# Performance work log

Measured on AMD Instinct MI355X. Metric: run time of the kernel, lower is better.

The kernel has to match this reference:

```python
import jax, jax.numpy as jnp
import numpy as np

KERNEL_MUL = 10.0
KERNEL_NUM = 5


def _multi_kernel(dist, n_samples):
    # bandwidth estimated from detached distances (torch uses .data)
    bw = jax.lax.stop_gradient(jnp.sum(dist)) / (n_samples * n_samples - n_samples)
    bw = bw / (KERNEL_MUL ** (KERNEL_NUM // 2))
    k = jnp.zeros_like(dist)
    for i in range(KERNEL_NUM):
        k = k + jnp.exp(-dist / (bw * KERNEL_MUL ** i))
    return k


def setup_inputs() -> dict:
    key = jax.random.key(0)
    k1, k2 = jax.random.split(key)
    B, D = 256, 512
    source = jax.random.normal(k1, (B, D), dtype=jnp.float32)
    target = jax.random.normal(k2, (B, D), dtype=jnp.float32)
    return {"source": source, "target": target}


def reference(source, target):
    B = source.shape[0]
    src = source.reshape(B, -1)
    tgt = target.reshape(target.shape[0], -1)
    total = jnp.concatenate([src, tgt], axis=0)  # [N, D], N = 2B
    N = total.shape[0]

    # L2 pairwise distances via norm expansion (avoids [N,N,D] intermediate)
    sq = jnp.sum(total * total, axis=1)  # [N]
    L2 = jnp.maximum(sq[:, None] + sq[None, :] - 2.0 * (total @ total.T), 0.0)

    # L1 pairwise distances (structurally needs pairwise diffs)
    L1 = jnp.sum(jnp.abs(total[:, None, :] - total[None, :, :]), axis=-1)  # [N, N]

    kernels = _multi_kernel(L2, N) + _multi_kernel(L1, N)

    XX = kernels[:B, :B]
    YY = kernels[B:, B:]
    XY = kernels[:B, B:]
    YX = kernels[B:, :B]
    return jnp.mean(XX + YY - XY - YX)
```

## Files before the change

### kernel.cpp

```cpp
#include <hip/hip_runtime.h>
#include <hip/hip_fp16.h>

#define NROWS 512
#define BHALF 256
#define DIM   512
#define TILE  64
#define DCHUNK 64
#define NCHUNK 8
#define NN (NROWS * NROWS)
#define SOFF (8 * NN)

#define ACC(A, Bb, IV, JV)                                    \
    {                                                         \
        const float d_ = (IV) - (JV);                         \
        a2[A][Bb] = fmaf(d_, d_, a2[A][Bb]);                  \
        a1[A][Bb] += fabsf(d_);                               \
    }

#define STEP(DD)                                              \
    {                                                         \
        const float4 ivv = *(const float4*)&ai[DD][ty4];      \
        const float4 jvv = *(const float4*)&aj[DD][tx4];      \
        ACC(0, 0, ivv.x, jvv.x) ACC(0, 1, ivv.x, jvv.y)       \
        ACC(0, 2, ivv.x, jvv.z) ACC(0, 3, ivv.x, jvv.w)       \
        ACC(1, 0, ivv.y, jvv.x) ACC(1, 1, ivv.y, jvv.y)       \
        ACC(1, 2, ivv.y, jvv.z) ACC(1, 3, ivv.y, jvv.w)       \
        ACC(2, 0, ivv.z, jvv.x) ACC(2, 1, ivv.z, jvv.y)       \
        ACC(2, 2, ivv.z, jvv.z) ACC(2, 3, ivv.z, jvv.w)       \
        ACC(3, 0, ivv.w, jvv.x) ACC(3, 1, ivv.w, jvv.y)       \
        ACC(3, 2, ivv.w, jvv.z) ACC(3, 3, ivv.w, jvv.w)       \
    }

__device__ __forceinline__ unsigned int pack_h2(float l2v, float l1v) {
    const __half2 h = __halves2half2(__float2half_rn(l2v), __float2half_rn(l1v));
    union { __half2 h; unsigned int u; } c; c.h = h;
    return c.u;
}

__global__ __launch_bounds__(256) void k_dist(const float* __restrict__ src,
                                              const float* __restrict__ tgt,
                                              float* __restrict__ ws,
                                              float* __restrict__ out)
{
    __shared__ float ai[DCHUNK][TILE];
    __shared__ float aj[DCHUNK][TILE];

    const int tj = blockIdx.x;
    const int ti = blockIdx.y;
    const int dc = blockIdx.z;
    const int t  = threadIdx.x;

    if (t == 0 && tj == 0 && ti == 0 && dc == 0) out[0] = 0.0f;

    {
        const int r  = t & 63;
        const int dg = t >> 6;
        const int gi = ti * TILE + r;
        const int gj = tj * TILE + r;
        const float* prow_i = (gi < BHALF ? src + (size_t)gi * DIM
                                          : tgt + (size_t)(gi - BHALF) * DIM) + dc * DCHUNK;
        const float* prow_j = (gj < BHALF ? src + (size_t)gj * DIM
                                          : tgt + (size_t)(gj - BHALF) * DIM) + dc * DCHUNK;
#pragma unroll
        for (int k = 0; k < 4; ++k) {
            const int d4 = dg * 4 + k;
            const float4 vi = *(const float4*)(prow_i + d4 * 4);
            const float4 vj = *(const float4*)(prow_j + d4 * 4);
            ai[d4 * 4 + 0][r] = vi.x; ai[d4 * 4 + 1][r] = vi.y;
            ai[d4 * 4 + 2][r] = vi.z; ai[d4 * 4 + 3][r] = vi.w;
            aj[d4 * 4 + 0][r] = vj.x; aj[d4 * 4 + 1][r] = vj.y;
            aj[d4 * 4 + 2][r] = vj.z; aj[d4 * 4 + 3][r] = vj.w;
        }
    }
    __syncthreads();

    const int tx  = t & 15;
    const int ty  = t >> 4;
    const int tx4 = tx * 4;
    const int ty4 = ty * 4;

    float a2[4][4], a1[4][4];
#pragma unroll
    for (int a = 0; a < 4; ++a)
#pragma unroll
        for (int b = 0; b < 4; ++b) { a2[a][b] = 0.f; a1[a][b] = 0.f; }

#pragma unroll 4
    for (int d = 0; d < DCHUNK; d += 2) {
        STEP(d)
        STEP(d + 1)
    }

    unsigned int* part = (unsigned int*)ws + (size_t)dc * NN;
    const int gj0 = tj * TILE + tx4;
#pragma unroll
    for (int a = 0; a < 4; ++a) {
        const int gi = ti * TILE + ty4 + a;
        const uint4 pk = make_uint4(pack_h2(a2[a][0], a1[a][0]),
                                    pack_h2(a2[a][1], a1[a][1]),
                                    pack_h2(a2[a][2], a1[a][2]),
                                    pack_h2(a2[a][3], a1[a][3]));
        *(uint4*)&part[(size_t)gi * NROWS + gj0] = pk;
    }

    float s2 = 0.f, s1 = 0.f;
#pragma unroll
    for (int a = 0; a < 4; ++a)
#pragma unroll
        for (int b = 0; b < 4; ++b) { s2 += a2[a][b]; s1 += a1[a][b]; }
#pragma unroll
    for (int off = 32; off > 0; off >>= 1) {
        s2 += __shfl_down(s2, off);
        s1 += __shfl_down(s1, off);
    }
    __syncthreads();
    float* red = &ai[0][0];
    const int wave = t >> 6;
    if ((t & 63) == 0) { red[wave * 2] = s2; red[wave * 2 + 1] = s1; }
    __syncthreads();
    if (t == 0) {
        const int bid = (dc * 8 + ti) * 8 + tj;
        ws[SOFF + bid]       = red[0] + red[2] + red[4] + red[6];
        ws[SOFF + 512 + bid] = red[1] + red[3] + red[5] + red[7];
    }
}

__global__ __launch_bounds__(256) void k_mmd(const float* __restrict__ ws,
                                             float* __restrict__ out)
{
    const int t = threadIdx.x;
    __shared__ float sred[8];

    float sp2 = ws[SOFF + t] + ws[SOFF + 256 + t];
    float sp1 = ws[SOFF + 512 + t] + ws[SOFF + 768 + t];
#pragma unroll
    for (int off = 32; off > 0; off >>= 1) {
        sp2 += __shfl_down(sp2, off);
        sp1 += __shfl_down(sp1, off);
    }
    if ((t & 63) == 0) { sred[(t >> 6) * 2] = sp2; sred[(t >> 6) * 2 + 1] = sp1; }
    __syncthreads();
    const float S2 = sred[0] + sred[2] + sred[4] + sred[6];
    const float S1 = sred[1] + sred[3] + sred[5] + sred[7];
    const float r2 = 26163200.0f / S2;
    const float r1 = 26163200.0f / S1;

    const __half2* part = (const __half2*)ws;

    float acc = 0.f;
    const int base = blockIdx.x * 1024 + t;
#pragma unroll
    for (int q = 0; q < 4; ++q) {
        const int idx = base + q * 256;
        float l2 = 0.f, l1 = 0.f;
#pragma unroll
        for (int c = 0; c < NCHUNK; ++c) {
            const float2 f = __half22float2(part[(size_t)c * NN + idx]);
            l2 += f.x;
            l1 += f.y;
        }
        float kv = 0.f;
        float f2 = r2, f1 = r1;
#pragma unroll
        for (int tt = 0; tt < 5; ++tt) {
            kv += __expf(-l2 * f2) + __expf(-l1 * f1);
            f2 *= 0.1f;
            f1 *= 0.1f;
        }
        const int i = idx >> 9;
        const int j = idx & 511;
        const float sgn = (((i ^ j) & BHALF) == 0) ? 1.0f : -1.0f;
        acc += sgn * kv;
    }
#pragma unroll
    for (int off = 32; off > 0; off >>= 1) acc += __shfl_down(acc, off);

    __syncthreads();
    if ((t & 63) == 0) sred[t >> 6] = acc;
    __syncthreads();
    if (t == 0) {
        const float s = sred[0] + sred[1] + sred[2] + sred[3];
        atomicAdd(out, s * (1.0f / 65536.0f));
    }
}

extern "C" void kernel_launch(void* const* d_in, const int* in_sizes, int n_in,
                              void* d_out, int out_size, void* d_ws, size_t ws_size,
                              hipStream_t stream)
{
    const float* src = (const float*)d_in[0];
    const float* tgt = (const float*)d_in[1];
    float* ws  = (float*)d_ws;
    float* out = (float*)d_out;

    dim3 g1(8, 8, 8);
    k_dist<<<g1, 256, 0, stream>>>(src, tgt, ws, out);
    k_mmd<<<256, 256, 0, stream>>>(ws, out);
}
```

Measured before the change: 78.82 us.

## Fuse distance and MMD kernels into one cooperative launch with grid sync

Merges the distance-partials kernel and the kernel-sum/MMD kernel into a single cooperative kernel that uses a grid-wide barrier between the phases. Each of the 512 blocks then reduces two adjacent pair elements per thread instead of the old 256-block layout with four per thread. This removes one kernel launch and the gap between launches. The cost is a grid sync, which requires all 512 blocks to be co-resident, and cooperative launch overhead.

New measurement: 129.8 us. 64.7% more time.

```diff
diff --git a/kernel.cpp b/kernel.cpp
--- a/kernel.cpp
+++ b/kernel.cpp
@@ -1,5 +1,8 @@
 #include <hip/hip_runtime.h>
 #include <hip/hip_fp16.h>
+#include <hip/hip_cooperative_groups.h>
+
+namespace cg = cooperative_groups;
 
 #define NROWS 512
 #define BHALF 256
@@ -37,10 +40,10 @@
     return c.u;
 }
 
-__global__ __launch_bounds__(256) void k_dist(const float* __restrict__ src,
-                                              const float* __restrict__ tgt,
-                                              float* __restrict__ ws,
-                                              float* __restrict__ out)
+__global__ __launch_bounds__(256) void k_fused(const float* __restrict__ src,
+                                               const float* __restrict__ tgt,
+                                               float* __restrict__ ws,
+                                               float* __restrict__ out)
 {
     __shared__ float ai[DCHUNK][TILE];
     __shared__ float aj[DCHUNK][TILE];
@@ -103,32 +106,31 @@
         *(uint4*)&part[(size_t)gi * NROWS + gj0] = pk;
     }
 
-    float s2 = 0.f, s1 = 0.f;
-#pragma unroll
-    for (int a = 0; a < 4; ++a)
-#pragma unroll
-        for (int b = 0; b < 4; ++b) { s2 += a2[a][b]; s1 += a1[a][b]; }
-#pragma unroll
-    for (int off = 32; off > 0; off >>= 1) {
-        s2 += __shfl_down(s2, off);
-        s1 += __shfl_down(s1, off);
-    }
-    __syncthreads();
-    float* red = &ai[0][0];
-    const int wave = t >> 6;
-    if ((t & 63) == 0) { red[wave * 2] = s2; red[wave * 2 + 1] = s1; }
-    __syncthreads();
-    if (t == 0) {
-        const int bid = (dc * 8 + ti) * 8 + tj;
-        ws[SOFF + bid]       = red[0] + red[2] + red[4] + red[6];
-        ws[SOFF + 512 + bid] = red[1] + red[3] + red[5] + red[7];
-    }
-}
-
-__global__ __launch_bounds__(256) void k_mmd(const float* __restrict__ ws,
-                                             float* __restrict__ out)
-{
-    const int t = threadIdx.x;
+    {
+        float s2 = 0.f, s1 = 0.f;
+#pragma unroll
+        for (int a = 0; a < 4; ++a)
+#pragma unroll
+            for (int b = 0; b < 4; ++b) { s2 += a2[a][b]; s1 += a1[a][b]; }
+#pragma unroll
+        for (int off = 32; off > 0; off >>= 1) {
+            s2 += __shfl_down(s2, off);
+            s1 += __shfl_down(s1, off);
+        }
+        __syncthreads();
+        float* red = &ai[0][0];
+        const int wave = t >> 6;
+        if ((t & 63) == 0) { red[wave * 2] = s2; red[wave * 2 + 1] = s1; }
+        __syncthreads();
+        if (t == 0) {
+            const int bid = (dc * 8 + ti) * 8 + tj;
+            ws[SOFF + bid]       = red[0] + red[2] + red[4] + red[6];
+            ws[SOFF + 512 + bid] = red[1] + red[3] + red[5] + red[7];
+        }
+    }
+
+    cg::this_grid().sync();
+
     __shared__ float sred[8];
 
     float sp2 = ws[SOFF + t] + ws[SOFF + 256 + t];
@@ -145,33 +147,37 @@
     const float r2 = 26163200.0f / S2;
     const float r1 = 26163200.0f / S1;
 
-    const __half2* part = (const __half2*)ws;
-
-    float acc = 0.f;
-    const int base = blockIdx.x * 1024 + t;
-#pragma unroll
-    for (int q = 0; q < 4; ++q) {
-        const int idx = base + q * 256;
-        float l2 = 0.f, l1 = 0.f;
-#pragma unroll
-        for (int c = 0; c < NCHUNK; ++c) {
-            const float2 f = __half22float2(part[(size_t)c * NN + idx]);
-            l2 += f.x;
-            l1 += f.y;
-        }
-        float kv = 0.f;
+    const int b = (blockIdx.z * 8 + blockIdx.y) * 8 + blockIdx.x;
+    const int p0 = (b * 256 + t) * 2;
+    const unsigned int* partr = (const unsigned int*)ws;
+
+    float l2a = 0.f, l1a = 0.f, l2b = 0.f, l1b = 0.f;
+#pragma unroll
+    for (int c = 0; c < NCHUNK; ++c) {
+        const uint2 w2 = *(const uint2*)&partr[(size_t)c * NN + p0];
+        union { unsigned int u; __half2 h; } ca, cb;
+        ca.u = w2.x; cb.u = w2.y;
+        const float2 fa = __half22float2(ca.h);
+        const float2 fb = __half22float2(cb.h);
+        l2a += fa.x; l1a += fa.y;
+        l2b += fb.x; l1b += fb.y;
+    }
+
+    float kv = 0.f;
+    {
         float f2 = r2, f1 = r1;
 #pragma unroll
         for (int tt = 0; tt < 5; ++tt) {
-            kv += __expf(-l2 * f2) + __expf(-l1 * f1);
+            kv += __expf(-l2a * f2) + __expf(-l1a * f1)
+                + __expf(-l2b * f2) + __expf(-l1b * f1);
             f2 *= 0.1f;
             f1 *= 0.1f;
         }
-        const int i = idx >> 9;
-        const int j = idx & 511;
-        const float sgn = (((i ^ j) & BHALF) == 0) ? 1.0f : -1.0f;
-        acc += sgn * kv;
-    }
+    }
+    const int i = p0 >> 9;
+    const int j = p0 & 511;
+    float acc = ((((i ^ j) & BHALF) == 0) ? kv : -kv);
+
 #pragma unroll
     for (int off = 32; off > 0; off >>= 1) acc += __shfl_down(acc, off);
 
@@ -193,7 +199,7 @@
     float* ws  = (float*)d_ws;
     float* out = (float*)d_out;
 
-    dim3 g1(8, 8, 8);
-    k_dist<<<g1, 256, 0, stream>>>(src, tgt, ws, out);
-    k_mmd<<<256, 256, 0, stream>>>(ws, out);
+    void* args[] = { (void*)&src, (void*)&tgt, (void*)&ws, (void*)&out };
+    hipLaunchCooperativeKernel((const void*)k_fused, dim3(8, 8, 8), dim3(256),
+                               args, 0, stream);
 }
```
